# Kernel tuning notes

Measured on AMD Instinct MI355X. Metric: run time of the kernel, lower is better.

The kernel has to match this reference:

```python
import jax, jax.numpy as jnp
import numpy as np

B, N, F_IN, F_OUT = 8, 2048, 256, 128
ALPHA = 0.2  # LeakyReLU negative slope
NEG_BIG = -9e15


def setup_inputs() -> dict:
    key = jax.random.key(0)
    k1, k2, k3, k4 = jax.random.split(key, 4)
    h = jax.random.normal(k1, (B, N, F_IN), dtype=jnp.float32)
    adj = jax.random.randint(k2, (B, N, N), 0, 2, dtype=jnp.int32)
    W = jax.random.normal(k3, (F_IN, F_OUT), dtype=jnp.float32) * 0.05
    a = jax.random.normal(k4, (2 * F_OUT,), dtype=jnp.float32) * 0.05
    return {"h": h, "adj": adj, "W": W, "a": a}


def reference(h, adj, W, a):
    # Wh: [B, N, F_OUT]
    Wh = jnp.einsum("bnf,fo->bno", h, W)
    # a([Wh_i || Wh_j]) decomposes: e_ij = a1.Wh_i + a2.Wh_j  (avoids [B,N*N,2F] tensor)
    a1, a2 = a[:F_OUT], a[F_OUT:]
    s1 = jnp.einsum("bno,o->bn", Wh, a1)  # [B, N]
    s2 = jnp.einsum("bno,o->bn", Wh, a2)  # [B, N]
    e = jax.nn.leaky_relu(s1[:, :, None] + s2[:, None, :], negative_slope=ALPHA)  # [B,N,N]
    e = jnp.where(adj > 0, e, NEG_BIG)
    attention = jax.nn.softmax(e, axis=2)
    # dropout is identity (eval / p=0)
    h_prime = jnp.einsum("bij,bjo->bio", attention, Wh)  # [B, N, F_OUT]
    return h_prime
```

## Files before the change

### kernel.cpp

```cpp
#include <hip/hip_runtime.h>

#define NB 8
#define NN 2048
#define FIN 256
#define FOUT 128

typedef __attribute__((ext_vector_type(8))) short short8;
typedef __attribute__((ext_vector_type(4))) float f32x4;

static __device__ __forceinline__ unsigned short f2bf(float f) {
    unsigned int u = __float_as_uint(f);
    u += 0x7fffu + ((u >> 16) & 1u);
    return (unsigned short)(u >> 16);
}

__global__ __launch_bounds__(256) void gat_prep(
    const float* __restrict__ h, const float* __restrict__ W, const float* __restrict__ a,
    unsigned short* __restrict__ whpv, float* __restrict__ s1g, float* __restrict__ s2g)
{
    __shared__ __align__(16) float hT[64 * FIN];
    __shared__ __align__(16) unsigned short pvs[8192];
    const int t = threadIdx.x;
    const int bx = blockIdx.x;
    const int b = bx >> 5;
    const int jt = bx & 31;
    const int j0 = jt * 64;

    const float* hsrc = h + ((size_t)b * NN + j0) * FIN;
    #pragma unroll
    for (int p = 0; p < 16; ++p) {
        int idx = p * 256 + t;
        *(f32x4*)&hT[idx * 4] = *(const f32x4*)&hsrc[idx * 4];
    }
    __syncthreads();

    const int cg = t & 31;
    const int rg = t >> 5;
    float acc[8][4];
    #pragma unroll
    for (int r = 0; r < 8; ++r)
        #pragma unroll
        for (int q = 0; q < 4; ++q) acc[r][q] = 0.f;

    for (int f = 0; f < FIN; f += 4) {
        f32x4 wv[4];
        #pragma unroll
        for (int q = 0; q < 4; ++q) wv[q] = *(const f32x4*)&W[(f + q) * FOUT + cg * 4];
        #pragma unroll
        for (int r = 0; r < 8; ++r) {
            f32x4 hv = *(const f32x4*)&hT[(rg * 8 + r) * FIN + f];
            #pragma unroll
            for (int q = 0; q < 4; ++q) {
                acc[r][0] += hv[q] * wv[q][0];
                acc[r][1] += hv[q] * wv[q][1];
                acc[r][2] += hv[q] * wv[q][2];
                acc[r][3] += hv[q] * wv[q][3];
            }
        }
    }

    f32x4 a1v = *(const f32x4*)&a[cg * 4];
    f32x4 a2v = *(const f32x4*)&a[FOUT + cg * 4];
    #pragma unroll
    for (int r = 0; r < 8; ++r) {
        float p1 = acc[r][0]*a1v[0] + acc[r][1]*a1v[1] + acc[r][2]*a1v[2] + acc[r][3]*a1v[3];
        float p2 = acc[r][0]*a2v[0] + acc[r][1]*a2v[1] + acc[r][2]*a2v[2] + acc[r][3]*a2v[3];
        #pragma unroll
        for (int m = 16; m >= 1; m >>= 1) {
            p1 += __shfl_xor(p1, m, 64);
            p2 += __shfl_xor(p2, m, 64);
        }
        if (cg == 0) {
            s1g[b * NN + j0 + rg * 8 + r] = p1;
            s2g[b * NN + j0 + rg * 8 + r] = p2;
        }
    }

    #pragma unroll
    for (int r = 0; r < 8; ++r) {
        int jl = rg * 8 + r;
        int kt = jl >> 5, j5 = jl & 31, g = j5 >> 3, i = j5 & 7;
        #pragma unroll
        for (int q = 0; q < 4; ++q) {
            int c = cg * 4 + q;
            int lane = g * 16 + (c & 15);
            int nt = c >> 4;
            pvs[((kt * 8 + nt) * 64 + lane) * 8 + i] = f2bf(acc[r][q]);
        }
    }
    __syncthreads();
    unsigned short* dst = whpv + (size_t)(b * 32 + jt) * 8192;
    #pragma unroll
    for (int p = 0; p < 4; ++p) {
        int idx = p * 2048 + t * 8;
        *(short8*)&dst[idx] = *(const short8*)&pvs[idx];
    }
}

__global__ __launch_bounds__(512, 4) void gat_main(
    const int* __restrict__ adj, const unsigned short* __restrict__ whpv,
    const float* __restrict__ s1g, const float* __restrict__ s2g, float* __restrict__ out)
{
    __shared__ __align__(16) char Plds[2][32 * 128];
    __shared__ __align__(16) unsigned short BL[2][8192];
    __shared__ float Sden[32];

    const int t = threadIdx.x;
    const int bx = blockIdx.x;
    const int b = bx >> 6;
    const int i0 = (bx & 63) * 32;

    const int r  = t >> 4;
    const int jq = t & 15;

    const int lane = t & 63;
    const int w = t >> 6;
    const int mt = w & 1;
    const int nb = w >> 1;
    const int arow = mt * 16 + (lane & 15);
    const int g = lane >> 4;

    const float s1v = s1g[b * NN + i0 + r];

    f32x4 acc[2];
    acc[0] = (f32x4){0.f, 0.f, 0.f, 0.f};
    acc[1] = (f32x4){0.f, 0.f, 0.f, 0.f};
    float ssum = 0.f;

    const int* adjb = adj + (size_t)b * NN * NN + (size_t)i0 * NN;
    const int* aptr = adjb + (size_t)r * NN + jq * 4;
    const unsigned short* whb = whpv + (size_t)b * 32 * 8192;
    const float* s2b = s2g + b * NN;

    int4 ac = *(const int4*)aptr;
    short8 wc0 = *(const short8*)&whb[t * 8];
    short8 wc1 = *(const short8*)&whb[4096 + t * 8];

    const int pbyte = r * 128 + ((jq >> 1) ^ (r & 7)) * 16 + (jq & 1) * 8;
    const int abyte = arow * 128;
    int buf = 0;

    for (int jc = 0; jc < 32; ++jc) {
        const int jn = (jc + 1) & 31;
        int4 an = *(const int4*)(aptr + jn * 64);
        const unsigned short* wn = whb + (size_t)jn * 8192;
        short8 wn0 = *(const short8*)&wn[t * 8];
        short8 wn1 = *(const short8*)&wn[4096 + t * 8];

        f32x4 s2v = *(const f32x4*)&s2b[jc * 64 + jq * 4];
        float p[4];
        {
            float e0 = s1v + s2v[0]; e0 = fmaxf(e0, 0.2f * e0);
            p[0] = (ac.x > 0) ? __expf(e0) : 0.f;
            float e1 = s1v + s2v[1]; e1 = fmaxf(e1, 0.2f * e1);
            p[1] = (ac.y > 0) ? __expf(e1) : 0.f;
            float e2 = s1v + s2v[2]; e2 = fmaxf(e2, 0.2f * e2);
            p[2] = (ac.z > 0) ? __expf(e2) : 0.f;
            float e3 = s1v + s2v[3]; e3 = fmaxf(e3, 0.2f * e3);
            p[3] = (ac.w > 0) ? __expf(e3) : 0.f;
        }
        ssum += (p[0] + p[1]) + (p[2] + p[3]);
        unsigned int pk0 = (unsigned int)f2bf(p[0]) | ((unsigned int)f2bf(p[1]) << 16);
        unsigned int pk1 = (unsigned int)f2bf(p[2]) | ((unsigned int)f2bf(p[3]) << 16);
        uint2 pk = {pk0, pk1};
        *(uint2*)&Plds[buf][pbyte] = pk;

        *(short8*)&BL[buf][t * 8] = wc0;
        *(short8*)&BL[buf][4096 + t * 8] = wc1;
        __syncthreads();

        #pragma unroll
        for (int kt = 0; kt < 2; ++kt) {
            int aslot = (4 * kt + g) ^ (arow & 7);
            short8 af = *(const short8*)&Plds[buf][abyte + aslot * 16];
            #pragma unroll
            for (int n = 0; n < 2; ++n) {
                int nt = nb * 2 + n;
                short8 bfr = *(const short8*)&BL[buf][((kt * 8 + nt) * 64 + lane) * 8];
                acc[n] = __builtin_amdgcn_mfma_f32_16x16x32_bf16(af, bfr, acc[n], 0, 0, 0);
            }
        }

        ac = an; wc0 = wn0; wc1 = wn1; buf ^= 1;
    }

    {
        float v = ssum;
        #pragma unroll
        for (int m = 8; m >= 1; m >>= 1) v += __shfl_xor(v, m, 64);
        if (jq == 0) Sden[r] = v;
    }
    __syncthreads();

    float* ob = out + ((size_t)b * NN + i0) * FOUT;
    #pragma unroll
    for (int n = 0; n < 2; ++n) {
        int col = (nb * 2 + n) * 16 + (lane & 15);
        #pragma unroll
        for (int q = 0; q < 4; ++q) {
            int row = mt * 16 + (lane >> 4) * 4 + q;
            ob[(size_t)row * FOUT + col] = acc[n][q] / Sden[row];
        }
    }
}

extern "C" void kernel_launch(void* const* d_in, const int* in_sizes, int n_in,
                              void* d_out, int out_size, void* d_ws, size_t ws_size,
                              hipStream_t stream) {
    (void)in_sizes; (void)n_in; (void)out_size; (void)ws_size;
    const float* h   = (const float*)d_in[0];
    const int*   adj = (const int*)d_in[1];
    const float* W   = (const float*)d_in[2];
    const float* a   = (const float*)d_in[3];
    float* out = (float*)d_out;

    unsigned short* whpv = (unsigned short*)d_ws;
    float* s1g = (float*)((char*)d_ws + (4u << 20));
    float* s2g = (float*)((char*)d_ws + (4u << 20) + (64u << 10));

    gat_prep<<<dim3(256), dim3(256), 0, stream>>>(h, W, a, whpv, s1g, s2g);
    gat_main<<<dim3(512), dim3(512), 0, stream>>>(adj, whpv, s1g, s2g, out);
}
```

Baseline: 79.47 us.

## Deepen global prefetch to two stages and use lgkm-only barrier in GAT main loop

Loads for adjacency, Wh tiles and s2 are now issued two iterations ahead using register double-buffering, with the loop unrolled by 2 so slot indices are static. The __syncthreads is replaced by an explicit lgkmcnt(0) wait plus s_barrier, so the barrier does not also wait on outstanding global loads (vmcnt). This is meant to hide HBM latency of the large adj stream. It uses more registers, which may pressure the occupancy target of 4 blocks, and the ordering now relies on the hand-written waitcnt placed before the barrier.

```diff
diff --git a/kernel.cpp b/kernel.cpp
--- a/kernel.cpp
+++ b/kernel.cpp
@@ -13,6 +13,14 @@
     u += 0x7fffu + ((u >> 16) & 1u);
     return (unsigned short)(u >> 16);
 }
+
+#define BAR_LGKM()                                            \
+    do {                                                      \
+        asm volatile("s_waitcnt lgkmcnt(0)" ::: "memory");    \
+        __builtin_amdgcn_sched_barrier(0);                    \
+        __builtin_amdgcn_s_barrier();                         \
+        __builtin_amdgcn_sched_barrier(0);                    \
+    } while (0)
 
 __global__ __launch_bounds__(256) void gat_prep(
     const float* __restrict__ h, const float* __restrict__ W, const float* __restrict__ a,
@@ -132,42 +140,58 @@
     const unsigned short* whb = whpv + (size_t)b * 32 * 8192;
     const float* s2b = s2g + b * NN;
 
-    int4 ac = *(const int4*)aptr;
-    short8 wc0 = *(const short8*)&whb[t * 8];
-    short8 wc1 = *(const short8*)&whb[4096 + t * 8];
+    int4   ac[2];
+    short8 wf0[2], wf1[2];
+    f32x4  s2r[2];
+    ac[0]  = *(const int4*)aptr;
+    wf0[0] = *(const short8*)&whb[t * 8];
+    wf1[0] = *(const short8*)&whb[4096 + t * 8];
+    s2r[0] = *(const f32x4*)&s2b[jq * 4];
+    ac[1]  = *(const int4*)(aptr + 64);
+    wf0[1] = *(const short8*)&whb[8192 + t * 8];
+    wf1[1] = *(const short8*)&whb[8192 + 4096 + t * 8];
+    s2r[1] = *(const f32x4*)&s2b[64 + jq * 4];
 
     const int pbyte = r * 128 + ((jq >> 1) ^ (r & 7)) * 16 + (jq & 1) * 8;
     const int abyte = arow * 128;
-    int buf = 0;
-
+
+    #pragma unroll 2
     for (int jc = 0; jc < 32; ++jc) {
-        const int jn = (jc + 1) & 31;
-        int4 an = *(const int4*)(aptr + jn * 64);
-        const unsigned short* wn = whb + (size_t)jn * 8192;
-        short8 wn0 = *(const short8*)&wn[t * 8];
-        short8 wn1 = *(const short8*)&wn[4096 + t * 8];
-
-        f32x4 s2v = *(const f32x4*)&s2b[jc * 64 + jq * 4];
-        float p[4];
+        const int slot = jc & 1;
+        const int buf  = jc & 1;
+
+        int4   a_  = ac[slot];
+        short8 wc0 = wf0[slot];
+        short8 wc1 = wf1[slot];
+        f32x4  s2v = s2r[slot];
+
+        const int jn = (jc + 2) & 31;
+        ac[slot]  = *(const int4*)(aptr + jn * 64);
+        wf0[slot] = *(const short8*)&whb[(size_t)jn * 8192 + t * 8];
+        wf1[slot] = *(const short8*)&whb[(size_t)jn * 8192 + 4096 + t * 8];
+        s2r[slot] = *(const f32x4*)&s2b[jn * 64 + jq * 4];
+
+        float p0, p1, p2, p3;
         {
             float e0 = s1v + s2v[0]; e0 = fmaxf(e0, 0.2f * e0);
-            p[0] = (ac.x > 0) ? __expf(e0) : 0.f;
+            p0 = (a_.x > 0) ? __expf(e0) : 0.f;
             float e1 = s1v + s2v[1]; e1 = fmaxf(e1, 0.2f * e1);
-            p[1] = (ac.y > 0) ? __expf(e1) : 0.f;
+            p1 = (a_.y > 0) ? __expf(e1) : 0.f;
             float e2 = s1v + s2v[2]; e2 = fmaxf(e2, 0.2f * e2);
-            p[2] = (ac.z > 0) ? __expf(e2) : 0.f;
+            p2 = (a_.z > 0) ? __expf(e2) : 0.f;
             float e3 = s1v + s2v[3]; e3 = fmaxf(e3, 0.2f * e3);
-            p[3] = (ac.w > 0) ? __expf(e3) : 0.f;
-        }
-        ssum += (p[0] + p[1]) + (p[2] + p[3]);
-        unsigned int pk0 = (unsigned int)f2bf(p[0]) | ((unsigned int)f2bf(p[1]) << 16);
-        unsigned int pk1 = (unsigned int)f2bf(p[2]) | ((unsigned int)f2bf(p[3]) << 16);
+            p3 = (a_.w > 0) ? __expf(e3) : 0.f;
+        }
+        ssum += (p0 + p1) + (p2 + p3);
+        unsigned int pk0 = (unsigned int)f2bf(p0) | ((unsigned int)f2bf(p1) << 16);
+        unsigned int pk1 = (unsigned int)f2bf(p2) | ((unsigned int)f2bf(p3) << 16);
         uint2 pk = {pk0, pk1};
         *(uint2*)&Plds[buf][pbyte] = pk;
 
         *(short8*)&BL[buf][t * 8] = wc0;
         *(short8*)&BL[buf][4096 + t * 8] = wc1;
-        __syncthreads();
+
+        BAR_LGKM();
 
         #pragma unroll
         for (int kt = 0; kt < 2; ++kt) {
@@ -180,8 +204,6 @@
                 acc[n] = __builtin_amdgcn_mfma_f32_16x16x32_bf16(af, bfr, acc[n], 0, 0, 0);
             }
         }
-
-        ac = an; wc0 = wn0; wc1 = wn1; buf ^= 1;
     }
 
     {
```

Measured after the change: 75.85 us. -4.6%, faster.

## Double row tile to 64 per block with 1024 threads and deeper prefetch

Applied to the files above, without the earlier changes.

The main kernel now handles 64 query rows per block with 1024 threads, so each Wh chunk staged into LDS is reused by twice as many rows and the grid halves to 256 blocks. It also interleaves blocks across batches, stages s2 in LDS, and prefetches adjacency and Wh two chunks ahead with nontemporal adj loads and output stores. The loop is manually unrolled with explicit lgkmcnt waits plus barriers around the MFMA phase. The costs are two barriers per chunk instead of one, higher register and LDS pressure per block, and only 256 blocks on the device.

```diff
diff --git a/kernel.cpp b/kernel.cpp
--- a/kernel.cpp
+++ b/kernel.cpp
@@ -7,12 +7,21 @@
 
 typedef __attribute__((ext_vector_type(8))) short short8;
 typedef __attribute__((ext_vector_type(4))) float f32x4;
+typedef __attribute__((ext_vector_type(4))) int i32x4;
 
 static __device__ __forceinline__ unsigned short f2bf(float f) {
     unsigned int u = __float_as_uint(f);
     u += 0x7fffu + ((u >> 16) & 1u);
     return (unsigned short)(u >> 16);
 }
+
+#define BAR_LGKM()                                            \
+    do {                                                      \
+        asm volatile("s_waitcnt lgkmcnt(0)" ::: "memory");    \
+        __builtin_amdgcn_sched_barrier(0);                    \
+        __builtin_amdgcn_s_barrier();                         \
+        __builtin_amdgcn_sched_barrier(0);                    \
+    } while (0)
 
 __global__ __launch_bounds__(256) void gat_prep(
     const float* __restrict__ h, const float* __restrict__ W, const float* __restrict__ a,
@@ -97,92 +106,104 @@
     }
 }
 
-__global__ __launch_bounds__(512, 4) void gat_main(
+__global__ __launch_bounds__(1024, 4) void gat_main(
     const int* __restrict__ adj, const unsigned short* __restrict__ whpv,
     const float* __restrict__ s1g, const float* __restrict__ s2g, float* __restrict__ out)
 {
-    __shared__ __align__(16) char Plds[2][32 * 128];
-    __shared__ __align__(16) unsigned short BL[2][8192];
-    __shared__ float Sden[32];
+    __shared__ __align__(16) char Plds[2][64 * 128];
+    __shared__ __align__(16) unsigned short Bl[2][8192];
+    __shared__ __align__(16) float s2s[NN];
+    __shared__ float Sden[64];
 
     const int t = threadIdx.x;
     const int bx = blockIdx.x;
-    const int b = bx >> 6;
-    const int i0 = (bx & 63) * 32;
+    const int b = bx & 7;
+    const int i0 = (bx >> 3) * 64;
 
     const int r  = t >> 4;
     const int jq = t & 15;
 
     const int lane = t & 63;
     const int w = t >> 6;
-    const int mt = w & 1;
-    const int nb = w >> 1;
-    const int arow = mt * 16 + (lane & 15);
+    const int mg = w >> 3;
+    const int ng = w & 7;
     const int g = lane >> 4;
-
+    const int c15 = lane & 15;
+
+    const float* s2b = s2g + b * NN;
     const float s1v = s1g[b * NN + i0 + r];
 
-    f32x4 acc[2];
-    acc[0] = (f32x4){0.f, 0.f, 0.f, 0.f};
-    acc[1] = (f32x4){0.f, 0.f, 0.f, 0.f};
+    const int* aptr = adj + (size_t)b * NN * NN + (size_t)(i0 + r) * NN + jq * 4;
+    const unsigned short* whb = whpv + (size_t)b * 32 * 8192;
+
+    float2 s2tmp = *(const float2*)&s2b[t * 2];
+
+    i32x4  adjv[2];
+    short8 whp[2];
+    adjv[0] = __builtin_nontemporal_load((const i32x4*)(aptr));
+    whp[0]  = *(const short8*)&whb[t * 8];
+    adjv[1] = __builtin_nontemporal_load((const i32x4*)(aptr + 64));
+    whp[1]  = *(const short8*)&whb[8192 + t * 8];
+
+    *(float2*)&s2s[t * 2] = s2tmp;
+
+    f32x4 acc0 = (f32x4){0.f, 0.f, 0.f, 0.f};
+    f32x4 acc1 = (f32x4){0.f, 0.f, 0.f, 0.f};
     float ssum = 0.f;
 
-    const int* adjb = adj + (size_t)b * NN * NN + (size_t)i0 * NN;
-    const int* aptr = adjb + (size_t)r * NN + jq * 4;
-    const unsigned short* whb = whpv + (size_t)b * 32 * 8192;
-    const float* s2b = s2g + b * NN;
-
-    int4 ac = *(const int4*)aptr;
-    short8 wc0 = *(const short8*)&whb[t * 8];
-    short8 wc1 = *(const short8*)&whb[4096 + t * 8];
-
     const int pbyte = r * 128 + ((jq >> 1) ^ (r & 7)) * 16 + (jq & 1) * 8;
-    const int abyte = arow * 128;
-    int buf = 0;
-
-    for (int jc = 0; jc < 32; ++jc) {
-        const int jn = (jc + 1) & 31;
-        int4 an = *(const int4*)(aptr + jn * 64);
-        const unsigned short* wn = whb + (size_t)jn * 8192;
-        short8 wn0 = *(const short8*)&wn[t * 8];
-        short8 wn1 = *(const short8*)&wn[4096 + t * 8];
-
-        f32x4 s2v = *(const f32x4*)&s2b[jc * 64 + jq * 4];
-        float p[4];
-        {
-            float e0 = s1v + s2v[0]; e0 = fmaxf(e0, 0.2f * e0);
-            p[0] = (ac.x > 0) ? __expf(e0) : 0.f;
-            float e1 = s1v + s2v[1]; e1 = fmaxf(e1, 0.2f * e1);
-            p[1] = (ac.y > 0) ? __expf(e1) : 0.f;
-            float e2 = s1v + s2v[2]; e2 = fmaxf(e2, 0.2f * e2);
-            p[2] = (ac.z > 0) ? __expf(e2) : 0.f;
-            float e3 = s1v + s2v[3]; e3 = fmaxf(e3, 0.2f * e3);
-            p[3] = (ac.w > 0) ? __expf(e3) : 0.f;
-        }
-        ssum += (p[0] + p[1]) + (p[2] + p[3]);
-        unsigned int pk0 = (unsigned int)f2bf(p[0]) | ((unsigned int)f2bf(p[1]) << 16);
-        unsigned int pk1 = (unsigned int)f2bf(p[2]) | ((unsigned int)f2bf(p[3]) << 16);
-        uint2 pk = {pk0, pk1};
-        *(uint2*)&Plds[buf][pbyte] = pk;
-
-        *(short8*)&BL[buf][t * 8] = wc0;
-        *(short8*)&BL[buf][4096 + t * 8] = wc1;
-        __syncthreads();
-
-        #pragma unroll
-        for (int kt = 0; kt < 2; ++kt) {
-            int aslot = (4 * kt + g) ^ (arow & 7);
-            short8 af = *(const short8*)&Plds[buf][abyte + aslot * 16];
-            #pragma unroll
-            for (int n = 0; n < 2; ++n) {
-                int nt = nb * 2 + n;
-                short8 bfr = *(const short8*)&BL[buf][((kt * 8 + nt) * 64 + lane) * 8];
-                acc[n] = __builtin_amdgcn_mfma_f32_16x16x32_bf16(af, bfr, acc[n], 0, 0, 0);
-            }
-        }
-
-        ac = an; wc0 = wn0; wc1 = wn1; buf ^= 1;
-    }
+    const int arow0 = mg * 32 + c15;
+    const int arow1 = mg * 32 + 16 + c15;
+    const int bsh0 = ((0 * 8 + ng) * 64 + lane) * 8;
+    const int bsh1 = ((1 * 8 + ng) * 64 + lane) * 8;
+
+    BAR_LGKM();
+
+#define GAT_BODY(S, JC)                                                         \
+    do {                                                                        \
+        i32x4  av = adjv[S];                                                    \
+        short8 wv = whp[S];                                                     \
+        const int jn = ((JC) + 2) & 31;                                         \
+        adjv[S] = __builtin_nontemporal_load((const i32x4*)(aptr + jn * 64));   \
+        whp[S]  = *(const short8*)&whb[(size_t)jn * 8192 + t * 8];              \
+        f32x4 s2v = *(const f32x4*)&s2s[(JC) * 64 + jq * 4];                    \
+        float e0 = s1v + s2v[0]; e0 = fmaxf(e0, 0.2f * e0);                     \
+        float p0 = (av.x > 0) ? __expf(e0) : 0.f;                               \
+        float e1 = s1v + s2v[1]; e1 = fmaxf(e1, 0.2f * e1);                     \
+        float p1 = (av.y > 0) ? __expf(e1) : 0.f;                               \
+        float e2 = s1v + s2v[2]; e2 = fmaxf(e2, 0.2f * e2);                     \
+        float p2 = (av.z > 0) ? __expf(e2) : 0.f;                               \
+        float e3 = s1v + s2v[3]; e3 = fmaxf(e3, 0.2f * e3);                     \
+        float p3 = (av.w > 0) ? __expf(e3) : 0.f;                               \
+        ssum += (p0 + p1) + (p2 + p3);                                          \
+        unsigned int pk0 = (unsigned int)f2bf(p0) | ((unsigned int)f2bf(p1) << 16); \
+        unsigned int pk1 = (unsigned int)f2bf(p2) | ((unsigned int)f2bf(p3) << 16); \
+        uint2 pk = {pk0, pk1};                                                  \
+        *(uint2*)&Plds[S][pbyte] = pk;                                          \
+        *(short8*)&Bl[S][t * 8] = wv;                                           \
+        BAR_LGKM();                                                             \
+        {                                                                       \
+            short8 bf0 = *(const short8*)&Bl[S][bsh0];                          \
+            int sl0 = (0 + g) ^ (arow0 & 7);                                    \
+            short8 af00 = *(const short8*)&Plds[S][arow0 * 128 + sl0 * 16];     \
+            short8 af01 = *(const short8*)&Plds[S][arow1 * 128 + sl0 * 16];     \
+            acc0 = __builtin_amdgcn_mfma_f32_16x16x32_bf16(af00, bf0, acc0, 0, 0, 0); \
+            acc1 = __builtin_amdgcn_mfma_f32_16x16x32_bf16(af01, bf0, acc1, 0, 0, 0); \
+            short8 bf1 = *(const short8*)&Bl[S][bsh1];                          \
+            int sl1 = (4 + g) ^ (arow0 & 7);                                    \
+            short8 af10 = *(const short8*)&Plds[S][arow0 * 128 + sl1 * 16];     \
+            short8 af11 = *(const short8*)&Plds[S][arow1 * 128 + sl1 * 16];     \
+            acc0 = __builtin_amdgcn_mfma_f32_16x16x32_bf16(af10, bf1, acc0, 0, 0, 0); \
+            acc1 = __builtin_amdgcn_mfma_f32_16x16x32_bf16(af11, bf1, acc1, 0, 0, 0); \
+        }                                                                       \
+        BAR_LGKM();                                                             \
+    } while (0)
+
+    for (int jc = 0; jc < 32; jc += 2) {
+        GAT_BODY(0, jc);
+        GAT_BODY(1, jc + 1);
+    }
+#undef GAT_BODY
 
     {
         float v = ssum;
@@ -193,14 +214,13 @@
     __syncthreads();
 
     float* ob = out + ((size_t)b * NN + i0) * FOUT;
-    #pragma unroll
-    for (int n = 0; n < 2; ++n) {
-        int col = (nb * 2 + n) * 16 + (lane & 15);
-        #pragma unroll
-        for (int q = 0; q < 4; ++q) {
-            int row = mt * 16 + (lane >> 4) * 4 + q;
-            ob[(size_t)row * FOUT + col] = acc[n][q] / Sden[row];
-        }
+    const int col = ng * 16 + c15;
+    #pragma unroll
+    for (int q = 0; q < 4; ++q) {
+        int row0 = mg * 32 + g * 4 + q;
+        int row1 = mg * 32 + 16 + g * 4 + q;
+        __builtin_nontemporal_store(acc0[q] / Sden[row0], &ob[(size_t)row0 * FOUT + col]);
+        __builtin_nontemporal_store(acc1[q] / Sden[row1], &ob[(size_t)row1 * FOUT + col]);
     }
 }
 
@@ -219,5 +239,5 @@
     float* s2g = (float*)((char*)d_ws + (4u << 20) + (64u << 10));
 
     gat_prep<<<dim3(256), dim3(256), 0, stream>>>(h, W, a, whpv, s1g, s2g);
-    gat_main<<<dim3(512), dim3(512), 0, stream>>>(adj, whpv, s1g, s2g, out);
-}
+    gat_main<<<dim3(256), dim3(1024), 0, stream>>>(adj, whpv, s1g, s2g, out);
+}
```

After: 68.63 us. 1.16x faster.

## Split key dimension across blocks with 128-row tiles and add combine kernel

Applied to the files above, without the earlier changes.

The main kernel now gives each block 128 query rows and a quarter of the key range (512 columns), instead of 32 rows over all 2048 keys. Each B fragment is reused across 8 MFMA column tiles, which cuts repeated Wh loads per block. Unnormalized partial outputs and row sums go to workspace, and a new combine kernel adds the four partials and divides by the softmax denominator. The change also adds nontemporal adjacency loads, stages s2 in LDS, and uses a custom barrier, at the cost of an extra launch plus 32MB of partial-result writes and reads.

```diff
diff --git a/kernel.cpp b/kernel.cpp
--- a/kernel.cpp
+++ b/kernel.cpp
@@ -7,12 +7,22 @@
 
 typedef __attribute__((ext_vector_type(8))) short short8;
 typedef __attribute__((ext_vector_type(4))) float f32x4;
+typedef __attribute__((ext_vector_type(4))) int i32x4;
+typedef __attribute__((ext_vector_type(4))) unsigned int u32x4;
 
 static __device__ __forceinline__ unsigned short f2bf(float f) {
     unsigned int u = __float_as_uint(f);
     u += 0x7fffu + ((u >> 16) & 1u);
     return (unsigned short)(u >> 16);
 }
+
+#define BAR_LGKM()                                            \
+    do {                                                      \
+        asm volatile("s_waitcnt lgkmcnt(0)" ::: "memory");    \
+        __builtin_amdgcn_sched_barrier(0);                    \
+        __builtin_amdgcn_s_barrier();                         \
+        __builtin_amdgcn_sched_barrier(0);                    \
+    } while (0)
 
 __global__ __launch_bounds__(256) void gat_prep(
     const float* __restrict__ h, const float* __restrict__ W, const float* __restrict__ a,
@@ -97,110 +107,170 @@
     }
 }
 
+static __device__ __forceinline__ uint2 pquad(i32x4 av, f32x4 s2v, float s1v, float& ssum) {
+    float e0 = s1v + s2v[0]; e0 = fmaxf(e0, 0.2f * e0);
+    float p0 = (av.x > 0) ? __expf(e0) : 0.f;
+    float e1 = s1v + s2v[1]; e1 = fmaxf(e1, 0.2f * e1);
+    float p1 = (av.y > 0) ? __expf(e1) : 0.f;
+    float e2 = s1v + s2v[2]; e2 = fmaxf(e2, 0.2f * e2);
+    float p2 = (av.z > 0) ? __expf(e2) : 0.f;
+    float e3 = s1v + s2v[3]; e3 = fmaxf(e3, 0.2f * e3);
+    float p3 = (av.w > 0) ? __expf(e3) : 0.f;
+    ssum += (p0 + p1) + (p2 + p3);
+    uint2 pk;
+    pk.x = (unsigned int)f2bf(p0) | ((unsigned int)f2bf(p1) << 16);
+    pk.y = (unsigned int)f2bf(p2) | ((unsigned int)f2bf(p3) << 16);
+    return pk;
+}
+
 __global__ __launch_bounds__(512, 4) void gat_main(
     const int* __restrict__ adj, const unsigned short* __restrict__ whpv,
-    const float* __restrict__ s1g, const float* __restrict__ s2g, float* __restrict__ out)
+    const float* __restrict__ s1g, const float* __restrict__ s2g,
+    float* __restrict__ part, float* __restrict__ spart)
 {
-    __shared__ __align__(16) char Plds[2][32 * 128];
-    __shared__ __align__(16) unsigned short BL[2][8192];
-    __shared__ float Sden[32];
+    __shared__ __align__(16) char Plds[2][128 * 128];
+    __shared__ __align__(16) unsigned short Bl[2][8192];
+    __shared__ __align__(16) float s2s[512];
 
     const int t = threadIdx.x;
     const int bx = blockIdx.x;
-    const int b = bx >> 6;
-    const int i0 = (bx & 63) * 32;
-
-    const int r  = t >> 4;
-    const int jq = t & 15;
+    const int b    = bx & 7;
+    const int rest = bx >> 3;
+    const int it   = rest & 15;
+    const int js   = rest >> 4;
+    const int i0 = it * 128;
+
+    const int r  = t >> 2;
+    const int q4 = t & 3;
 
     const int lane = t & 63;
     const int w = t >> 6;
-    const int mt = w & 1;
-    const int nb = w >> 1;
-    const int arow = mt * 16 + (lane & 15);
     const int g = lane >> 4;
+    const int c15 = lane & 15;
+
+    s2s[t] = s2g[b * NN + js * 512 + t];
 
     const float s1v = s1g[b * NN + i0 + r];
-
-    f32x4 acc[2];
-    acc[0] = (f32x4){0.f, 0.f, 0.f, 0.f};
-    acc[1] = (f32x4){0.f, 0.f, 0.f, 0.f};
+    const int* aptr = adj + (size_t)b * NN * NN + (size_t)(i0 + r) * NN + js * 512 + q4 * 16;
+    const unsigned short* whb = whpv + (size_t)b * 32 * 8192 + (size_t)js * 8 * 8192;
+
+    f32x4 acc[8];
+    #pragma unroll
+    for (int nt = 0; nt < 8; ++nt) acc[nt] = (f32x4){0.f, 0.f, 0.f, 0.f};
     float ssum = 0.f;
 
-    const int* adjb = adj + (size_t)b * NN * NN + (size_t)i0 * NN;
-    const int* aptr = adjb + (size_t)r * NN + jq * 4;
-    const unsigned short* whb = whpv + (size_t)b * 32 * 8192;
-    const float* s2b = s2g + b * NN;
-
-    int4 ac = *(const int4*)aptr;
-    short8 wc0 = *(const short8*)&whb[t * 8];
-    short8 wc1 = *(const short8*)&whb[4096 + t * 8];
-
-    const int pbyte = r * 128 + ((jq >> 1) ^ (r & 7)) * 16 + (jq & 1) * 8;
-    const int abyte = arow * 128;
-    int buf = 0;
-
-    for (int jc = 0; jc < 32; ++jc) {
-        const int jn = (jc + 1) & 31;
-        int4 an = *(const int4*)(aptr + jn * 64);
-        const unsigned short* wn = whb + (size_t)jn * 8192;
-        short8 wn0 = *(const short8*)&wn[t * 8];
-        short8 wn1 = *(const short8*)&wn[4096 + t * 8];
-
-        f32x4 s2v = *(const f32x4*)&s2b[jc * 64 + jq * 4];
-        float p[4];
-        {
-            float e0 = s1v + s2v[0]; e0 = fmaxf(e0, 0.2f * e0);
-            p[0] = (ac.x > 0) ? __expf(e0) : 0.f;
-            float e1 = s1v + s2v[1]; e1 = fmaxf(e1, 0.2f * e1);
-            p[1] = (ac.y > 0) ? __expf(e1) : 0.f;
-            float e2 = s1v + s2v[2]; e2 = fmaxf(e2, 0.2f * e2);
-            p[2] = (ac.z > 0) ? __expf(e2) : 0.f;
-            float e3 = s1v + s2v[3]; e3 = fmaxf(e3, 0.2f * e3);
-            p[3] = (ac.w > 0) ? __expf(e3) : 0.f;
-        }
-        ssum += (p[0] + p[1]) + (p[2] + p[3]);
-        unsigned int pk0 = (unsigned int)f2bf(p[0]) | ((unsigned int)f2bf(p[1]) << 16);
-        unsigned int pk1 = (unsigned int)f2bf(p[2]) | ((unsigned int)f2bf(p[3]) << 16);
-        uint2 pk = {pk0, pk1};
-        *(uint2*)&Plds[buf][pbyte] = pk;
-
-        *(short8*)&BL[buf][t * 8] = wc0;
-        *(short8*)&BL[buf][4096 + t * 8] = wc1;
-        __syncthreads();
+    i32x4 a0 = __builtin_nontemporal_load((const i32x4*)(aptr));
+    i32x4 a1 = __builtin_nontemporal_load((const i32x4*)(aptr + 4));
+    i32x4 a2 = __builtin_nontemporal_load((const i32x4*)(aptr + 8));
+    i32x4 a3 = __builtin_nontemporal_load((const i32x4*)(aptr + 12));
+    short8 bc0 = *(const short8*)&whb[t * 16];
+    short8 bc1 = *(const short8*)&whb[t * 16 + 8];
+
+    __syncthreads();
+
+    const int arow = w * 16 + c15;
+
+    #pragma unroll 1
+    for (int c = 0; c < 8; ++c) {
+        const int buf = c & 1;
+        const int cn = (c + 1) & 7;
+
+        i32x4 n0 = __builtin_nontemporal_load((const i32x4*)(aptr + cn * 64));
+        i32x4 n1 = __builtin_nontemporal_load((const i32x4*)(aptr + cn * 64 + 4));
+        i32x4 n2 = __builtin_nontemporal_load((const i32x4*)(aptr + cn * 64 + 8));
+        i32x4 n3 = __builtin_nontemporal_load((const i32x4*)(aptr + cn * 64 + 12));
+        short8 bn0 = *(const short8*)&whb[(size_t)cn * 8192 + t * 16];
+        short8 bn1 = *(const short8*)&whb[(size_t)cn * 8192 + t * 16 + 8];
+
+        const int sb = c * 64 + q4 * 16;
+        uint2 pk0 = pquad(a0, *(const f32x4*)&s2s[sb],      s1v, ssum);
+        uint2 pk1 = pquad(a1, *(const f32x4*)&s2s[sb + 4],  s1v, ssum);
+        uint2 pk2 = pquad(a2, *(const f32x4*)&s2s[sb + 8],  s1v, ssum);
+        uint2 pk3 = pquad(a3, *(const f32x4*)&s2s[sb + 12], s1v, ssum);
+
+        u32x4 w0 = {pk0.x, pk0.y, pk1.x, pk1.y};
+        u32x4 w1 = {pk2.x, pk2.y, pk3.x, pk3.y};
+        const int sl0 = (q4 * 2)     ^ (r & 7);
+        const int sl1 = (q4 * 2 + 1) ^ (r & 7);
+        *(u32x4*)&Plds[buf][r * 128 + sl0 * 16] = w0;
+        *(u32x4*)&Plds[buf][r * 128 + sl1 * 16] = w1;
+
+        *(short8*)&Bl[buf][t * 16] = bc0;
+        *(short8*)&Bl[buf][t * 16 + 8] = bc1;
+
+        BAR_LGKM();
 
         #pragma unroll
         for (int kt = 0; kt < 2; ++kt) {
-            int aslot = (4 * kt + g) ^ (arow & 7);
-            short8 af = *(const short8*)&Plds[buf][abyte + aslot * 16];
+            const int aslot = (4 * kt + g) ^ (arow & 7);
+            short8 af = *(const short8*)&Plds[buf][arow * 128 + aslot * 16];
             #pragma unroll
-            for (int n = 0; n < 2; ++n) {
-                int nt = nb * 2 + n;
-                short8 bfr = *(const short8*)&BL[buf][((kt * 8 + nt) * 64 + lane) * 8];
-                acc[n] = __builtin_amdgcn_mfma_f32_16x16x32_bf16(af, bfr, acc[n], 0, 0, 0);
+            for (int nt = 0; nt < 8; ++nt) {
+                short8 bfr = *(const short8*)&Bl[buf][((kt * 8 + nt) * 64 + lane) * 8];
+                acc[nt] = __builtin_amdgcn_mfma_f32_16x16x32_bf16(af, bfr, acc[nt], 0, 0, 0);
             }
         }
 
-        ac = an; wc0 = wn0; wc1 = wn1; buf ^= 1;
+        a0 = n0; a1 = n1; a2 = n2; a3 = n3; bc0 = bn0; bc1 = bn1;
     }
 
     {
         float v = ssum;
-        #pragma unroll
-        for (int m = 8; m >= 1; m >>= 1) v += __shfl_xor(v, m, 64);
-        if (jq == 0) Sden[r] = v;
-    }
-    __syncthreads();
-
-    float* ob = out + ((size_t)b * NN + i0) * FOUT;
-    #pragma unroll
-    for (int n = 0; n < 2; ++n) {
-        int col = (nb * 2 + n) * 16 + (lane & 15);
+        v += __shfl_xor(v, 1, 64);
+        v += __shfl_xor(v, 2, 64);
+        if (q4 == 0) spart[(size_t)bx * 128 + r] = v;
+    }
+
+    float* pb = part + (size_t)bx * 16384;
+    #pragma unroll
+    for (int nt = 0; nt < 8; ++nt) {
+        const int col = nt * 16 + c15;
         #pragma unroll
         for (int q = 0; q < 4; ++q) {
-            int row = mt * 16 + (lane >> 4) * 4 + q;
-            ob[(size_t)row * FOUT + col] = acc[n][q] / Sden[row];
-        }
+            const int row = w * 16 + g * 4 + q;
+            pb[row * 128 + col] = acc[nt][q];
+        }
+    }
+}
+
+__global__ __launch_bounds__(256) void gat_combine(
+    const float* __restrict__ part, const float* __restrict__ spart,
+    float* __restrict__ out)
+{
+    const int t = threadIdx.x;
+    const int bc = blockIdx.x;
+    const int b   = bc & 7;
+    const int seg = bc >> 3;
+    const int it  = seg >> 2;
+    const int r0  = (seg & 3) * 32;
+
+    const int cq = t & 31;
+    const int rg = t >> 5;
+
+    size_t pb[4];
+    const float* sp[4];
+    #pragma unroll
+    for (int js = 0; js < 4; ++js) {
+        const int bxm = b + 8 * (it + 16 * js);
+        pb[js] = (size_t)bxm * 16384;
+        sp[js] = spart + (size_t)bxm * 128;
+    }
+
+    float* ob = out + ((size_t)b * NN + it * 128) * FOUT;
+
+    #pragma unroll
+    for (int rr = 0; rr < 4; ++rr) {
+        const int row = r0 + rg * 4 + rr;
+        const float sden = sp[0][row] + sp[1][row] + sp[2][row] + sp[3][row];
+        const float inv = 1.0f / sden;
+        const size_t off = (size_t)row * 128 + cq * 4;
+        f32x4 v0 = *(const f32x4*)&part[pb[0] + off];
+        f32x4 v1 = *(const f32x4*)&part[pb[1] + off];
+        f32x4 v2 = *(const f32x4*)&part[pb[2] + off];
+        f32x4 v3 = *(const f32x4*)&part[pb[3] + off];
+        f32x4 s = (v0 + v1) + (v2 + v3);
+        s[0] *= inv; s[1] *= inv; s[2] *= inv; s[3] *= inv;
+        *(f32x4*)&ob[off] = s;
     }
 }
 
@@ -215,9 +285,12 @@
     float* out = (float*)d_out;
 
     unsigned short* whpv = (unsigned short*)d_ws;
-    float* s1g = (float*)((char*)d_ws + (4u << 20));
-    float* s2g = (float*)((char*)d_ws + (4u << 20) + (64u << 10));
+    float* s1g  = (float*)((char*)d_ws + (4u << 20));
+    float* s2g  = (float*)((char*)d_ws + (4u << 20) + (64u << 10));
+    float* part = (float*)((char*)d_ws + (8u << 20));
+    float* spart= (float*)((char*)d_ws + (40u << 20));
 
     gat_prep<<<dim3(256), dim3(256), 0, stream>>>(h, W, a, whpv, s1g, s2g);
-    gat_main<<<dim3(512), dim3(512), 0, stream>>>(adj, whpv, s1g, s2g, out);
-}
+    gat_main<<<dim3(512), dim3(512), 0, stream>>>(adj, whpv, s1g, s2g, part, spart);
+    gat_combine<<<dim3(512), dim3(256), 0, stream>>>(part, spart, out);
+}
```

Measured after the change: 99.11 us. 1.25x slower.
